# Optimization experiments

Hardware: AMD Instinct MI355X
Metric: run time of the kernel (lower is better)

Reference implementation:

```python
import jax, jax.numpy as jnp
import numpy as np

B, T, C, H = 4, 2048, 768, 12
D = C // H

def setup_inputs() -> dict:
    key = jax.random.key(0)
    ks = jax.random.split(key, 8)
    s = 1.0 / np.sqrt(C)
    return {
        "x":  jax.random.normal(ks[0], (B, T, C), dtype=jnp.float32),
        "Wq": jax.random.normal(ks[1], (C, C), dtype=jnp.float32) * s,
        "bq": jax.random.normal(ks[2], (C,), dtype=jnp.float32) * 0.02,
        "Wk": jax.random.normal(ks[3], (C, C), dtype=jnp.float32) * s,
        "bk": jax.random.normal(ks[4], (C,), dtype=jnp.float32) * 0.02,
        "Wv": jax.random.normal(ks[5], (C, C), dtype=jnp.float32) * s,
        "bv": jax.random.normal(ks[6], (C,), dtype=jnp.float32) * 0.02,
        "Wp": jax.random.normal(ks[7], (C, C), dtype=jnp.float32) * s,
    }

def reference(x, Wq, bq, Wk, bk, Wv, bv, Wp):
    # Linear projections (torch Linear: y = x @ W.T + b)
    q = x @ Wq.T + bq
    k = x @ Wk.T + bk
    v = x @ Wv.T + bv
    # [B,T,C] -> [B,H,T,D]
    q = q.reshape(B, T, H, D).transpose(0, 2, 1, 3)
    k = k.reshape(B, T, H, D).transpose(0, 2, 1, 3)
    v = v.reshape(B, T, H, D).transpose(0, 2, 1, 3)
    scale = 1.0 / np.sqrt(D).astype(np.float32)
    scores = jnp.einsum('bhqd,bhkd->bhqk', q, k) * scale  # [B,H,T,T]
    attn = jax.nn.softmax(scores, axis=-1)  # no mask in original module
    out = jnp.einsum('bhqk,bhkd->bhqd', attn, v)
    out = out.transpose(0, 2, 1, 3).reshape(B, T, C)
    return out @ Wp.T  # proj has bias=False
```

## Files before the change

kernel.cpp:

```cpp
#include <hip/hip_runtime.h>
#include <hip/hip_bf16.h>
#include <cmath>

constexpr int B  = 4;
constexpr int T  = 2048;
constexpr int C  = 768;
constexpr int H  = 12;
constexpr int Dh = 64;
constexpr int M  = B * T;
constexpr int NQKV = 3 * C;
constexpr int WS2  = C * C;

typedef short bf16x8 __attribute__((ext_vector_type(8)));
typedef short bf16x4 __attribute__((ext_vector_type(4)));
typedef float f32x4  __attribute__((ext_vector_type(4)));

__device__ inline short f2bf(float f) {
    unsigned u = __float_as_uint(f);
    u += 0x7fffu + ((u >> 16) & 1u);
    return (short)(u >> 16);
}

__device__ inline unsigned pk_bf16(float a, float b) {
    __hip_bfloat162 h = __float22bfloat162_rn(float2{a, b});
    return *(unsigned*)&h;
}

typedef const __attribute__((address_space(1))) unsigned GU;
typedef __attribute__((address_space(3))) unsigned LU;
__device__ inline void async_copy16(const void* g, void* l) {
    __builtin_amdgcn_global_load_lds((GU*)g, (LU*)l, 16, 0, 0);
}

constexpr size_t XE = (size_t)M * C;
constexpr size_t CV_TOTAL = XE + 4 * (size_t)WS2;

__global__ __launch_bounds__(256)
void convert_all(const float* __restrict__ x,  const float* __restrict__ Wq,
                 const float* __restrict__ Wk, const float* __restrict__ Wv,
                 const float* __restrict__ Wp,
                 short* __restrict__ xb, short* __restrict__ Wqkv,
                 short* __restrict__ Wpb) {
    size_t i = ((size_t)blockIdx.x * 256 + threadIdx.x) * 4;
    const float* src; short* dst; size_t off;
    if (i < XE)                        { src = x;  dst = xb;            off = i; }
    else if (i < XE + WS2)             { src = Wq; dst = Wqkv;          off = i - XE; }
    else if (i < XE + 2 * (size_t)WS2) { src = Wk; dst = Wqkv + WS2;    off = i - XE - WS2; }
    else if (i < XE + 3 * (size_t)WS2) { src = Wv; dst = Wqkv + 2 * WS2; off = i - XE - 2 * (size_t)WS2; }
    else                               { src = Wp; dst = Wpb;           off = i - XE - 3 * (size_t)WS2; }
    float4 v = *(const float4*)(src + off);
    bf16x4 o; o[0] = f2bf(v.x); o[1] = f2bf(v.y); o[2] = f2bf(v.z); o[3] = f2bf(v.w);
    *(bf16x4*)(dst + off) = o;
}

constexpr int BM = 128, BK = 32;

template<int BN_, int WMW, int WNW, int OUT_BF16>
__global__ __launch_bounds__(256)
void gemm_bt(const short* __restrict__ A, const short* __restrict__ W,
             const float* __restrict__ bias0, const float* __restrict__ bias1,
             const float* __restrict__ bias2,
             void* __restrict__ Yv, int Ndim, int Kdim) {
    constexpr int MT = BM / WMW / 16;
    constexpr int NT = BN_ / WNW / 16;
    constexpr int NCHUNK = (BM + BN_) / 16;
    __shared__ short As[BM * BK];
    __shared__ short Bs[BN_ * BK];

    const int tid  = threadIdx.x;
    const int wave = tid >> 6;
    const int lane = tid & 63;
    const int li   = lane & 15;
    const int quad = lane >> 4;
    const int wm   = wave % WMW;
    const int wn   = wave / WMW;
    const int m0   = blockIdx.y * BM;
    const int n0   = blockIdx.x * BN_;

    f32x4 acc[MT][NT];
    #pragma unroll
    for (int i = 0; i < MT; ++i)
        #pragma unroll
        for (int j = 0; j < NT; ++j)
            acc[i][j] = (f32x4){0.f, 0.f, 0.f, 0.f};

    const int lrow = lane >> 2;
    const int lkof = (lane & 3) * 8;

    for (int k0 = 0; k0 < Kdim; k0 += BK) {
        __syncthreads();
        #pragma unroll
        for (int ii = 0; ii < NCHUNK / 4; ++ii) {
            int c = ii * 4 + wave;
            if (c < BM / 16)
                async_copy16(A + (size_t)(m0 + c * 16 + lrow) * Kdim + k0 + lkof,
                             &As[c * 512]);
            else
                async_copy16(W + (size_t)(n0 + (c - BM / 16) * 16 + lrow) * Kdim + k0 + lkof,
                             &Bs[(c - BM / 16) * 512]);
        }
        __syncthreads();

        bf16x8 af[MT], bfr[NT];
        #pragma unroll
        for (int t = 0; t < MT; ++t)
            af[t] = *(const bf16x8*)&As[(wm * MT * 16 + t * 16 + li) * BK + quad * 8];
        #pragma unroll
        for (int t = 0; t < NT; ++t)
            bfr[t] = *(const bf16x8*)&Bs[(wn * NT * 16 + t * 16 + li) * BK + quad * 8];
        #pragma unroll
        for (int i = 0; i < MT; ++i)
            #pragma unroll
            for (int j = 0; j < NT; ++j)
                acc[i][j] = __builtin_amdgcn_mfma_f32_16x16x32_bf16(
                    af[i], bfr[j], acc[i][j], 0, 0, 0);
    }

    float bb[NT];
    #pragma unroll
    for (int nt = 0; nt < NT; ++nt) bb[nt] = 0.f;
    if (bias0) {
        int s = n0 / C;
        const float* bp = (s == 0) ? bias0 : ((s == 1) ? bias1 : bias2);
        int nb = n0 % C;
        #pragma unroll
        for (int nt = 0; nt < NT; ++nt)
            bb[nt] = bp[nb + wn * NT * 16 + nt * 16 + li];
    }

    #pragma unroll
    for (int mt = 0; mt < MT; ++mt)
        #pragma unroll
        for (int nt = 0; nt < NT; ++nt)
            #pragma unroll
            for (int r = 0; r < 4; ++r) {
                int row = m0 + wm * MT * 16 + mt * 16 + quad * 4 + r;
                int col = n0 + wn * NT * 16 + nt * 16 + li;
                float v = acc[mt][nt][r] + bb[nt];
                if constexpr (OUT_BF16)
                    ((short*)Yv)[(size_t)row * Ndim + col] = f2bf(v);
                else
                    ((float*)Yv)[(size_t)row * Ndim + col] = v;
            }
}

constexpr int QT   = 128;
constexpr int KTT  = 64;
constexpr int LSTR = 72;
constexpr int PSTR = 72;
constexpr int QS   = NQKV;
constexpr float SOFT_SCALE = 0.18033688011112042f;

__global__ __launch_bounds__(256)
void attn_fwd(const short* __restrict__ QKV, short* __restrict__ O) {
    __shared__ short Ks[KTT * LSTR];
    __shared__ short Vt[Dh * LSTR];
    __shared__ short Ps[4 * 32 * PSTR];

    const int tid  = threadIdx.x;
    const int wave = tid >> 6;
    const int lane = tid & 63;
    const int li   = lane & 15;
    const int quad = lane >> 4;
    const int b    = blockIdx.z;
    const int h    = blockIdx.y;
    const int qw   = blockIdx.x * QT + wave * 32;

    const short* Qg = QKV + (size_t)(b * T) * QS + h * Dh;
    const short* Kg = QKV + (size_t)(b * T) * QS + C + h * Dh;
    const short* Vg = QKV + (size_t)(b * T) * QS + 2 * C + h * Dh;

    bf16x8 qf[2][2];
    #pragma unroll
    for (int qb = 0; qb < 2; ++qb)
        #pragma unroll
        for (int dh = 0; dh < 2; ++dh)
            qf[qb][dh] = *(const bf16x8*)(Qg + (size_t)(qw + qb * 16 + li) * QS
                                             + dh * 32 + quad * 8);

    bf16x8 ones;
    #pragma unroll
    for (int i = 0; i < 8; ++i) ones[i] = (short)0x3F80;

    f32x4 oacc[2][4];
    #pragma unroll
    for (int qb = 0; qb < 2; ++qb)
        #pragma unroll
        for (int db = 0; db < 4; ++db)
            oacc[qb][db] = (f32x4){0.f, 0.f, 0.f, 0.f};
    f32x4 lacc[2] = {(f32x4){0.f, 0.f, 0.f, 0.f}, (f32x4){0.f, 0.f, 0.f, 0.f}};

    const int ktok = tid >> 3;
    const int kch  = tid & 7;
    const int vd2  = (tid & 31) * 2;
    const int vg   = tid >> 5;

    int4 kpre[2];
    unsigned vpre[8];
    kpre[0] = *(const int4*)(Kg + (size_t)(ktok)      * QS + kch * 8);
    kpre[1] = *(const int4*)(Kg + (size_t)(ktok + 32) * QS + kch * 8);
    #pragma unroll
    for (int t2 = 0; t2 < 8; ++t2)
        vpre[t2] = *(const unsigned*)(Vg + (size_t)(vg * 8 + t2) * QS + vd2);

    for (int kt = 0; kt < T; kt += KTT) {
        __syncthreads();

        *(int4*)&Ks[ktok * LSTR + kch * 8]        = kpre[0];
        *(int4*)&Ks[(ktok + 32) * LSTR + kch * 8] = kpre[1];
        {
            unsigned lo[4], hi[4];
            #pragma unroll
            for (int j = 0; j < 4; ++j) {
                lo[j] = __builtin_amdgcn_perm(vpre[2 * j + 1], vpre[2 * j], 0x05040100u);
                hi[j] = __builtin_amdgcn_perm(vpre[2 * j + 1], vpre[2 * j], 0x07060302u);
            }
            *(int4*)&Vt[vd2 * LSTR + vg * 8]       = make_int4(lo[0], lo[1], lo[2], lo[3]);
            *(int4*)&Vt[(vd2 + 1) * LSTR + vg * 8] = make_int4(hi[0], hi[1], hi[2], hi[3]);
        }
        __syncthreads();

        if (kt + KTT < T) {
            const size_t nb = kt + KTT;
            kpre[0] = *(const int4*)(Kg + (nb + ktok)      * QS + kch * 8);
            kpre[1] = *(const int4*)(Kg + (nb + ktok + 32) * QS + kch * 8);
            #pragma unroll
            for (int t2 = 0; t2 < 8; ++t2)
                vpre[t2] = *(const unsigned*)(Vg + (nb + vg * 8 + t2) * QS + vd2);
        }

        f32x4 st[2][4];
        #pragma unroll
        for (int kb = 0; kb < 4; ++kb) {
            bf16x8 kf0 = *(const bf16x8*)&Ks[(kb * 16 + li) * LSTR + quad * 8];
            bf16x8 kf1 = *(const bf16x8*)&Ks[(kb * 16 + li) * LSTR + 32 + quad * 8];
            #pragma unroll
            for (int qb = 0; qb < 2; ++qb) {
                f32x4 a = (f32x4){0.f, 0.f, 0.f, 0.f};
                a = __builtin_amdgcn_mfma_f32_16x16x32_bf16(kf0, qf[qb][0], a, 0, 0, 0);
                a = __builtin_amdgcn_mfma_f32_16x16x32_bf16(kf1, qf[qb][1], a, 0, 0, 0);
                st[qb][kb] = a;
            }
        }

        #pragma unroll
        for (int qb = 0; qb < 2; ++qb)
            #pragma unroll
            for (int kb = 0; kb < 4; ++kb) {
                float p0 = __builtin_amdgcn_exp2f(st[qb][kb][0] * SOFT_SCALE);
                float p1 = __builtin_amdgcn_exp2f(st[qb][kb][1] * SOFT_SCALE);
                float p2 = __builtin_amdgcn_exp2f(st[qb][kb][2] * SOFT_SCALE);
                float p3 = __builtin_amdgcn_exp2f(st[qb][kb][3] * SOFT_SCALE);
                uint2 w; w.x = pk_bf16(p0, p1); w.y = pk_bf16(p2, p3);
                *(uint2*)&Ps[(wave * 32 + qb * 16 + li) * PSTR + kb * 16 + quad * 4] = w;
            }
        __asm__ volatile("s_waitcnt lgkmcnt(0)" ::: "memory");

        #pragma unroll
        for (int kq = 0; kq < 2; ++kq) {
            bf16x8 pf[2];
            #pragma unroll
            for (int qb = 0; qb < 2; ++qb) {
                pf[qb] = *(const bf16x8*)&Ps[(wave * 32 + qb * 16 + li) * PSTR
                                             + kq * 32 + quad * 8];
                lacc[qb] = __builtin_amdgcn_mfma_f32_16x16x32_bf16(
                    pf[qb], ones, lacc[qb], 0, 0, 0);
            }
            #pragma unroll
            for (int db = 0; db < 4; ++db) {
                bf16x8 vf = *(const bf16x8*)&Vt[(db * 16 + li) * LSTR + kq * 32 + quad * 8];
                #pragma unroll
                for (int qb = 0; qb < 2; ++qb)
                    oacc[qb][db] = __builtin_amdgcn_mfma_f32_16x16x32_bf16(
                        pf[qb], vf, oacc[qb][db], 0, 0, 0);
            }
        }
    }

    #pragma unroll
    for (int qb = 0; qb < 2; ++qb)
        #pragma unroll
        for (int r = 0; r < 4; ++r) {
            float inv = 1.0f / lacc[qb][r];
            short* op = O + (size_t)(b * T + qw + qb * 16 + quad * 4 + r) * C
                          + h * Dh + li;
            #pragma unroll
            for (int db = 0; db < 4; ++db)
                op[db * 16] = f2bf(oacc[qb][db][r] * inv);
        }
}

extern "C" void kernel_launch(void* const* d_in, const int* in_sizes, int n_in,
                              void* d_out, int out_size, void* d_ws, size_t ws_size,
                              hipStream_t stream) {
    (void)in_sizes; (void)n_in; (void)out_size; (void)ws_size;

    const float* x  = (const float*)d_in[0];
    const float* Wq = (const float*)d_in[1];
    const float* bq = (const float*)d_in[2];
    const float* Wk = (const float*)d_in[3];
    const float* bk = (const float*)d_in[4];
    const float* Wv = (const float*)d_in[5];
    const float* bv = (const float*)d_in[6];
    const float* Wp = (const float*)d_in[7];
    float* out = (float*)d_out;

    short* xb    = (short*)d_ws;
    short* Wqkv  = xb + (size_t)M * C;
    short* Wpb   = Wqkv + 3 * (size_t)WS2;
    short* QKVb  = Wpb + (size_t)WS2;
    short* AOb   = QKVb + (size_t)M * NQKV;

    convert_all<<<dim3(CV_TOTAL / 1024), 256, 0, stream>>>(
        x, Wq, Wk, Wv, Wp, xb, Wqkv, Wpb);

    gemm_bt<128, 2, 2, 1><<<dim3(NQKV / 128, M / BM), 256, 0, stream>>>(
        xb, Wqkv, bq, bk, bv, QKVb, NQKV, C);

    attn_fwd<<<dim3(T / QT, H, B), 256, 0, stream>>>(QKVb, AOb);

    gemm_bt<64, 4, 1, 0><<<dim3(C / 64, M / BM), 256, 0, stream>>>(
        AOb, Wpb, nullptr, nullptr, nullptr, out, C, C);
}
```

Measured before the change: 247.5 us.

## Register-prefetch GEMM tiles and double K-tile depth to 64

Replaces the direct global-to-LDS async copies in the bf16 GEMM with register prefetching. The next K tile is loaded into registers while MFMAs run on the current LDS tile, and the K tile grows from 32 to 64 so each barrier pair covers twice as many MFMAs. The goal is to hide global load latency and cut synchronisation overhead. In exchange it uses more registers and LDS, and the row stride of 64 bf16 may cause LDS bank conflicts on the fragment reads.

```diff
diff --git a/kernel.cpp b/kernel.cpp
--- a/kernel.cpp
+++ b/kernel.cpp
@@ -24,12 +24,6 @@
 __device__ inline unsigned pk_bf16(float a, float b) {
     __hip_bfloat162 h = __float22bfloat162_rn(float2{a, b});
     return *(unsigned*)&h;
-}
-
-typedef const __attribute__((address_space(1))) unsigned GU;
-typedef __attribute__((address_space(3))) unsigned LU;
-__device__ inline void async_copy16(const void* g, void* l) {
-    __builtin_amdgcn_global_load_lds((GU*)g, (LU*)l, 16, 0, 0);
 }
 
 constexpr size_t XE = (size_t)M * C;
@@ -53,7 +47,7 @@
     *(bf16x4*)(dst + off) = o;
 }
 
-constexpr int BM = 128, BK = 32;
+constexpr int BM = 128, BK2 = 64;
 
 template<int BN_, int WMW, int WNW, int OUT_BF16>
 __global__ __launch_bounds__(256)
@@ -63,9 +57,12 @@
              void* __restrict__ Yv, int Ndim, int Kdim) {
     constexpr int MT = BM / WMW / 16;
     constexpr int NT = BN_ / WNW / 16;
-    constexpr int NCHUNK = (BM + BN_) / 16;
-    __shared__ short As[BM * BK];
-    __shared__ short Bs[BN_ * BK];
+    constexpr int NA = BM * BK2 / 8;
+    constexpr int NTOT = (BM + BN_) * BK2 / 8;
+    constexpr int CH = NTOT / 256;
+
+    __shared__ short As[BM * BK2];
+    __shared__ short Bs[BN_ * BK2];
 
     const int tid  = threadIdx.x;
     const int wave = tid >> 6;
@@ -84,36 +81,57 @@
         for (int j = 0; j < NT; ++j)
             acc[i][j] = (f32x4){0.f, 0.f, 0.f, 0.f};
 
-    const int lrow = lane >> 2;
-    const int lkof = (lane & 3) * 8;
-
-    for (int k0 = 0; k0 < Kdim; k0 += BK) {
+    const short* gsrc[CH];
+    short* ldst[CH];
+    #pragma unroll
+    for (int i = 0; i < CH; ++i) {
+        int idx = i * 256 + tid;
+        if (idx < NA) {
+            int row = idx >> 3, ch = idx & 7;
+            gsrc[i] = A + (size_t)(m0 + row) * Kdim + ch * 8;
+            ldst[i] = &As[row * BK2 + ch * 8];
+        } else {
+            int idx2 = idx - NA;
+            int row = idx2 >> 3, ch = idx2 & 7;
+            gsrc[i] = W + (size_t)(n0 + row) * Kdim + ch * 8;
+            ldst[i] = &Bs[row * BK2 + ch * 8];
+        }
+    }
+
+    int4 pre[CH];
+    #pragma unroll
+    for (int i = 0; i < CH; ++i) pre[i] = *(const int4*)(gsrc[i]);
+
+    for (int k0 = 0; k0 < Kdim; k0 += BK2) {
         __syncthreads();
         #pragma unroll
-        for (int ii = 0; ii < NCHUNK / 4; ++ii) {
-            int c = ii * 4 + wave;
-            if (c < BM / 16)
-                async_copy16(A + (size_t)(m0 + c * 16 + lrow) * Kdim + k0 + lkof,
-                             &As[c * 512]);
-            else
-                async_copy16(W + (size_t)(n0 + (c - BM / 16) * 16 + lrow) * Kdim + k0 + lkof,
-                             &Bs[(c - BM / 16) * 512]);
-        }
+        for (int i = 0; i < CH; ++i) *(int4*)(ldst[i]) = pre[i];
         __syncthreads();
 
-        bf16x8 af[MT], bfr[NT];
-        #pragma unroll
-        for (int t = 0; t < MT; ++t)
-            af[t] = *(const bf16x8*)&As[(wm * MT * 16 + t * 16 + li) * BK + quad * 8];
-        #pragma unroll
-        for (int t = 0; t < NT; ++t)
-            bfr[t] = *(const bf16x8*)&Bs[(wn * NT * 16 + t * 16 + li) * BK + quad * 8];
-        #pragma unroll
-        for (int i = 0; i < MT; ++i)
-            #pragma unroll
-            for (int j = 0; j < NT; ++j)
-                acc[i][j] = __builtin_amdgcn_mfma_f32_16x16x32_bf16(
-                    af[i], bfr[j], acc[i][j], 0, 0, 0);
+        if (k0 + BK2 < Kdim) {
+            #pragma unroll
+            for (int i = 0; i < CH; ++i)
+                pre[i] = *(const int4*)(gsrc[i] + k0 + BK2);
+        }
+
+        #pragma unroll
+        for (int h = 0; h < 2; ++h) {
+            bf16x8 af[MT], bfr[NT];
+            #pragma unroll
+            for (int t = 0; t < MT; ++t)
+                af[t] = *(const bf16x8*)&As[(wm * MT * 16 + t * 16 + li) * BK2
+                                            + h * 32 + quad * 8];
+            #pragma unroll
+            for (int t = 0; t < NT; ++t)
+                bfr[t] = *(const bf16x8*)&Bs[(wn * NT * 16 + t * 16 + li) * BK2
+                                             + h * 32 + quad * 8];
+            #pragma unroll
+            for (int i = 0; i < MT; ++i)
+                #pragma unroll
+                for (int j = 0; j < NT; ++j)
+                    acc[i][j] = __builtin_amdgcn_mfma_f32_16x16x32_bf16(
+                        af[i], bfr[j], acc[i][j], 0, 0, 0);
+        }
     }
 
     float bb[NT];
```

New measurement: 388.9 us. 57.2% more time.
